# Kernel optimization log

Measured on AMD Instinct MI355X. Metric: run time of the kernel, lower is better.

## Reference

```python
import jax, jax.numpy as jnp
import numpy as np


def setup_inputs() -> dict:
    key = jax.random.key(0)
    k1, k2, k3, k4 = jax.random.split(key, 4)
    d_in, d_out, r = 4096, 4096, 16
    n_tok = 8192  # batch 4 * seq 2048
    x = jax.random.normal(k1, (n_tok, d_in), dtype=jnp.float32)
    W = jax.random.normal(k2, (d_out, d_in), dtype=jnp.float32)
    A = jax.random.normal(k3, (d_out, r), dtype=jnp.float32)
    B = jax.random.normal(k4, (r, d_in), dtype=jnp.float32)
    return {"x": x, "W": W, "A": A, "B": B}


def reference(x, W, A, B):
    # Faithful to torch: F.linear(x, W + A @ B) = x @ (W + A @ B)^T, no bias.
    W_eff = W + A @ B  # [d_out, d_in], materialized as in the original module
    return x @ W_eff.T  # [n_tok, d_out]
```

## Files before the change

kernel.cpp:

```cpp
#include <hip/hip_runtime.h>

typedef __attribute__((ext_vector_type(8))) short short8;
typedef __attribute__((ext_vector_type(4))) float f32x4;
typedef unsigned short ushort_t;

#define BAR()   __builtin_amdgcn_s_barrier()
#define LGKM0() asm volatile("s_waitcnt lgkmcnt(0)" ::: "memory")
#define VM6()   asm volatile("s_waitcnt vmcnt(6)" ::: "memory")
#define VM0()   asm volatile("s_waitcnt vmcnt(0)" ::: "memory")
#define PRIO(n) __builtin_amdgcn_s_setprio(n)
#define MFMA(a_, b_, c_) __builtin_amdgcn_mfma_f32_16x16x32_bf16(a_, b_, c_, 0, 0, 0)

__device__ __forceinline__ unsigned short f2bf(float f) {
  unsigned u = __builtin_bit_cast(unsigned, f);
  u += 0x7FFFu + ((u >> 16) & 1u);
  return (unsigned short)(u >> 16);
}

__device__ __forceinline__ void gl_lds16(const void* g, void* l) {
  __builtin_amdgcn_global_load_lds(
      (const __attribute__((address_space(1))) void*)g,
      (__attribute__((address_space(3))) void*)l, 16, 0, 0);
}

__global__ __launch_bounds__(256) void cvt_x(const float* __restrict__ x,
                                             ushort_t* __restrict__ xb) {
  size_t i = ((size_t)blockIdx.x * 256 + threadIdx.x) * 8;
  float4 v0 = *(const float4*)(x + i);
  float4 v1 = *(const float4*)(x + i + 4);
  union { ushort_t s[8]; uint4 v; } o;
  o.s[0] = f2bf(v0.x); o.s[1] = f2bf(v0.y); o.s[2] = f2bf(v0.z); o.s[3] = f2bf(v0.w);
  o.s[4] = f2bf(v1.x); o.s[5] = f2bf(v1.y); o.s[6] = f2bf(v1.z); o.s[7] = f2bf(v1.w);
  *(uint4*)(xb + i) = o.v;
}

__global__ __launch_bounds__(256) void build_weff(const float* __restrict__ W,
                                                  const float* __restrict__ A,
                                                  const float* __restrict__ B,
                                                  ushort_t* __restrict__ Weff) {
  const int K = 4096, R = 16;
  const int n = blockIdx.y;
  const int k = (blockIdx.x * 256 + threadIdx.x) * 8;
  float4 w0 = *(const float4*)(W + (size_t)n * K + k);
  float4 w1 = *(const float4*)(W + (size_t)n * K + k + 4);
  float s0 = w0.x, s1 = w0.y, s2 = w0.z, s3 = w0.w;
  float s4 = w1.x, s5 = w1.y, s6 = w1.z, s7 = w1.w;
#pragma unroll
  for (int r = 0; r < R; ++r) {
    float a = A[n * R + r];
    float4 b0 = *(const float4*)(B + (size_t)r * K + k);
    float4 b1 = *(const float4*)(B + (size_t)r * K + k + 4);
    s0 += a * b0.x; s1 += a * b0.y; s2 += a * b0.z; s3 += a * b0.w;
    s4 += a * b1.x; s5 += a * b1.y; s6 += a * b1.z; s7 += a * b1.w;
  }
  union { ushort_t s[8]; uint4 v; } o;
  o.s[0] = f2bf(s0); o.s[1] = f2bf(s1); o.s[2] = f2bf(s2); o.s[3] = f2bf(s3);
  o.s[4] = f2bf(s4); o.s[5] = f2bf(s5); o.s[6] = f2bf(s6); o.s[7] = f2bf(s7);
  *(uint4*)(Weff + (size_t)n * K + k) = o.v;
}


__device__ __forceinline__ void stage_half(const ushort_t* __restrict__ G, int row0, int kc,
                                           ushort_t* half, int tid) {
#pragma unroll
  for (int r = 0; r < 2; ++r) {
    const int idx  = r * 512 + tid;
    const int lrow = idx >> 2;
    const int cb   = ((idx & 3) * 16) ^ (((lrow >> 3) & 1) << 5);
    const ushort_t* src = G + (size_t)(row0 + lrow) * 4096 + kc + (cb >> 1);
    char* dst = (char*)half + (size_t)(r * 512 + (tid & ~63)) * 16;
    gl_lds16(src, dst);
  }
}

__global__ __launch_bounds__(512, 2) void gemm256(const ushort_t* __restrict__ Xb,
                                                  const ushort_t* __restrict__ Wb,
                                                  float* __restrict__ C) {
  const int N = 4096;
  const int NT = 4096 / 64;
  __shared__ __align__(16) ushort_t lds[2][4][256 * 32];

  const int tid = threadIdx.x;
  const int l   = tid & 63;
  const int w   = tid >> 6;
  const int wm  = w >> 2;
  const int wn  = w & 3;

  const int bid = blockIdx.x;
  const int c = bid & 7, q = bid >> 3;
  const int tm = (c >> 1) * 8 + (q >> 3);
  const int tn = (c & 1) * 8 + (q & 7);
  const int bm = tm * 256, bn = tn * 256;

  const int colb = ((l >> 4) * 16) ^ (((l >> 3) & 1) << 5);
  int aoff[8], boff[4];
#pragma unroll
  for (int mi = 0; mi < 8; ++mi) aoff[mi] = (wm * 128 + mi * 16 + (l & 15)) * 64 + colb;
#pragma unroll
  for (int ni = 0; ni < 4; ++ni) boff[ni] = (wn * 64 + ni * 16 + (l & 15)) * 64 + colb;

  f32x4 acc[8][4];
#pragma unroll
  for (int i = 0; i < 8; ++i)
#pragma unroll
    for (int j = 0; j < 4; ++j) acc[i][j] = (f32x4)(0.0f);

  stage_half(Wb, bn, 0,  lds[0][2], tid);
  stage_half(Xb, bm, 0,  lds[0][0], tid);
  stage_half(Wb, bn, 32, lds[0][3], tid);
  stage_half(Xb, bm, 32, lds[0][1], tid);
  stage_half(Wb, bn, 64, lds[1][2], tid);
  stage_half(Xb, bm, 64, lds[1][0], tid);
  stage_half(Wb, bn, 96, lds[1][3], tid);
  VM6();
  BAR();

  short8 af0, af1, af2, af3, bf0, bf1, bf2, bf3;

#define LDA(P_, I0_) do { \
    af0 = *(const short8*)((const char*)(P_) + aoff[(I0_) + 0]); \
    af1 = *(const short8*)((const char*)(P_) + aoff[(I0_) + 1]); \
    af2 = *(const short8*)((const char*)(P_) + aoff[(I0_) + 2]); \
    af3 = *(const short8*)((const char*)(P_) + aoff[(I0_) + 3]); \
  } while (0)
#define LDB(P_) do { \
    bf0 = *(const short8*)((const char*)(P_) + boff[0]); \
    bf1 = *(const short8*)((const char*)(P_) + boff[1]); \
    bf2 = *(const short8*)((const char*)(P_) + boff[2]); \
    bf3 = *(const short8*)((const char*)(P_) + boff[3]); \
  } while (0)
#define QUAD(M0_) do { \
    acc[(M0_)+0][0] = MFMA(af0, bf0, acc[(M0_)+0][0]); \
    acc[(M0_)+0][1] = MFMA(af0, bf1, acc[(M0_)+0][1]); \
    acc[(M0_)+0][2] = MFMA(af0, bf2, acc[(M0_)+0][2]); \
    acc[(M0_)+0][3] = MFMA(af0, bf3, acc[(M0_)+0][3]); \
    acc[(M0_)+1][0] = MFMA(af1, bf0, acc[(M0_)+1][0]); \
    acc[(M0_)+1][1] = MFMA(af1, bf1, acc[(M0_)+1][1]); \
    acc[(M0_)+1][2] = MFMA(af1, bf2, acc[(M0_)+1][2]); \
    acc[(M0_)+1][3] = MFMA(af1, bf3, acc[(M0_)+1][3]); \
    acc[(M0_)+2][0] = MFMA(af2, bf0, acc[(M0_)+2][0]); \
    acc[(M0_)+2][1] = MFMA(af2, bf1, acc[(M0_)+2][1]); \
    acc[(M0_)+2][2] = MFMA(af2, bf2, acc[(M0_)+2][2]); \
    acc[(M0_)+2][3] = MFMA(af2, bf3, acc[(M0_)+2][3]); \
    acc[(M0_)+3][0] = MFMA(af3, bf0, acc[(M0_)+3][0]); \
    acc[(M0_)+3][1] = MFMA(af3, bf1, acc[(M0_)+3][1]); \
    acc[(M0_)+3][2] = MFMA(af3, bf2, acc[(M0_)+3][2]); \
    acc[(M0_)+3][3] = MFMA(af3, bf3, acc[(M0_)+3][3]); \
  } while (0)

  int cur = 0;
  for (int t = 0; t < NT; ++t) {
    const ushort_t* A0h = lds[cur][0];
    const ushort_t* A1h = lds[cur][1];
    const ushort_t* B0h = lds[cur][2];
    const ushort_t* B1h = lds[cur][3];
    const int kc2 = (t + 2) * 64;

    LDA(A0h, 0); LDB(B0h);
    if (t + 1 < NT) stage_half(Xb, bm, (t + 1) * 64 + 32, lds[cur ^ 1][1], tid);
    BAR(); LGKM0(); PRIO(1);
    QUAD(0);
    PRIO(0); BAR();

    LDA(A0h, 4);
    if (t + 2 < NT) stage_half(Wb, bn, kc2, lds[cur][2], tid);
    BAR(); LGKM0(); PRIO(1);
    QUAD(4);
    PRIO(0); BAR();

    LDA(A1h, 0); LDB(B1h);
    if (t + 2 < NT) stage_half(Xb, bm, kc2, lds[cur][0], tid);
    BAR(); LGKM0(); PRIO(1);
    QUAD(0);
    PRIO(0); BAR();

    LDA(A1h, 4);
    if (t + 2 < NT) stage_half(Wb, bn, kc2 + 32, lds[cur][3], tid);
    if (t + 2 < NT) { VM6(); } else { VM0(); }
    BAR(); LGKM0(); PRIO(1);
    QUAD(4);
    PRIO(0); BAR();

    cur ^= 1;
  }

  const int erow = bm + wm * 128 + (l >> 4) * 4;
  const int ecol = bn + wn * 64 + (l & 15);
#pragma unroll
  for (int mi = 0; mi < 8; ++mi) {
#pragma unroll
    for (int ni = 0; ni < 4; ++ni) {
      float* cp = C + (size_t)(erow + mi * 16) * N + ecol + ni * 16;
#pragma unroll
      for (int j = 0; j < 4; ++j) cp[(size_t)j * N] = acc[mi][ni][j];
    }
  }
}

extern "C" void kernel_launch(void* const* d_in, const int* in_sizes, int n_in,
                              void* d_out, int out_size, void* d_ws, size_t ws_size,
                              hipStream_t stream) {
  const float* x = (const float*)d_in[0];
  const float* W = (const float*)d_in[1];
  const float* A = (const float*)d_in[2];
  const float* B = (const float*)d_in[3];
  float* out = (float*)d_out;

  ushort_t* xb = (ushort_t*)d_ws;
  ushort_t* wb = (ushort_t*)((char*)d_ws + (size_t)8192 * 4096 * 2);

  cvt_x<<<16384, 256, 0, stream>>>(x, xb);
  dim3 gw(2, 4096);
  build_weff<<<gw, 256, 0, stream>>>(W, A, B, wb);
  gemm256<<<512, 512, 0, stream>>>(xb, wb, out);
}
```

Measured before the change: 354.5 us.

## Simplify GEMM pipeline to single-stage K=32 double buffer with full vmcnt waits

Replaces the deeper staggered prefetch schedule (K=64 tiles split into halves, staged two iterations ahead with vmcnt(6)) with a simple double buffer over K=32 tiles, prefetching the next tile and waiting with vmcnt(0) at the end of each iteration. LDS use halves to 64 KB and the occupancy hint of 2 blocks per CU is dropped from launch_bounds. This cuts LDS footprint and barrier count per K step but exposes global-load latency more, since each tile load must finish within one short compute phase.

```diff
diff --git a/kernel.cpp b/kernel.cpp
--- a/kernel.cpp
+++ b/kernel.cpp
@@ -6,7 +6,6 @@
 
 #define BAR()   __builtin_amdgcn_s_barrier()
 #define LGKM0() asm volatile("s_waitcnt lgkmcnt(0)" ::: "memory")
-#define VM6()   asm volatile("s_waitcnt vmcnt(6)" ::: "memory")
 #define VM0()   asm volatile("s_waitcnt vmcnt(0)" ::: "memory")
 #define PRIO(n) __builtin_amdgcn_s_setprio(n)
 #define MFMA(a_, b_, c_) __builtin_amdgcn_mfma_f32_16x16x32_bf16(a_, b_, c_, 0, 0, 0)
@@ -73,12 +72,12 @@
   }
 }
 
-__global__ __launch_bounds__(512, 2) void gemm256(const ushort_t* __restrict__ Xb,
-                                                  const ushort_t* __restrict__ Wb,
-                                                  float* __restrict__ C) {
+__global__ __launch_bounds__(512) void gemm256(const ushort_t* __restrict__ Xb,
+                                               const ushort_t* __restrict__ Wb,
+                                               float* __restrict__ C) {
   const int N = 4096;
-  const int NT = 4096 / 64;
-  __shared__ __align__(16) ushort_t lds[2][4][256 * 32];
+  const int NT = 4096 / 32;
+  __shared__ __align__(16) ushort_t lds[2][2][256 * 32];
 
   const int tid = threadIdx.x;
   const int l   = tid & 63;
@@ -105,14 +104,9 @@
 #pragma unroll
     for (int j = 0; j < 4; ++j) acc[i][j] = (f32x4)(0.0f);
 
-  stage_half(Wb, bn, 0,  lds[0][2], tid);
-  stage_half(Xb, bm, 0,  lds[0][0], tid);
-  stage_half(Wb, bn, 32, lds[0][3], tid);
-  stage_half(Xb, bm, 32, lds[0][1], tid);
-  stage_half(Wb, bn, 64, lds[1][2], tid);
-  stage_half(Xb, bm, 64, lds[1][0], tid);
-  stage_half(Wb, bn, 96, lds[1][3], tid);
-  VM6();
+  stage_half(Xb, bm, 0, lds[0][0], tid);
+  stage_half(Wb, bn, 0, lds[0][1], tid);
+  VM0();
   BAR();
 
   short8 af0, af1, af2, af3, bf0, bf1, bf2, bf3;
@@ -150,37 +144,25 @@
 
   int cur = 0;
   for (int t = 0; t < NT; ++t) {
-    const ushort_t* A0h = lds[cur][0];
-    const ushort_t* A1h = lds[cur][1];
-    const ushort_t* B0h = lds[cur][2];
-    const ushort_t* B1h = lds[cur][3];
-    const int kc2 = (t + 2) * 64;
+    const ushort_t* Ah = lds[cur][0];
+    const ushort_t* Bh = lds[cur][1];
 
-    LDA(A0h, 0); LDB(B0h);
-    if (t + 1 < NT) stage_half(Xb, bm, (t + 1) * 64 + 32, lds[cur ^ 1][1], tid);
+    LDA(Ah, 0); LDB(Bh);
+    if (t + 1 < NT) {
+      const int kc = (t + 1) * 32;
+      stage_half(Xb, bm, kc, lds[cur ^ 1][0], tid);
+      stage_half(Wb, bn, kc, lds[cur ^ 1][1], tid);
+    }
     BAR(); LGKM0(); PRIO(1);
     QUAD(0);
     PRIO(0); BAR();
 
-    LDA(A0h, 4);
-    if (t + 2 < NT) stage_half(Wb, bn, kc2, lds[cur][2], tid);
+    LDA(Ah, 4);
     BAR(); LGKM0(); PRIO(1);
     QUAD(4);
-    PRIO(0); BAR();
-
-    LDA(A1h, 0); LDB(B1h);
-    if (t + 2 < NT) stage_half(Xb, bm, kc2, lds[cur][0], tid);
-    BAR(); LGKM0(); PRIO(1);
-    QUAD(0);
-    PRIO(0); BAR();
-
-    LDA(A1h, 4);
-    if (t + 2 < NT) stage_half(Wb, bn, kc2 + 32, lds[cur][3], tid);
-    if (t + 2 < NT) { VM6(); } else { VM0(); }
-    BAR(); LGKM0(); PRIO(1);
-    QUAD(4);
-    PRIO(0); BAR();
-
+    PRIO(0);
+    VM0();
+    BAR();
     cur ^= 1;
   }
 
```

After: 370.0 us. 1.04x slower.
